# Optimization experiments

Measured on AMD Instinct MI355X. Metric: run time of the kernel, lower is better.

## Reference

```python
import jax, jax.numpy as jnp
import numpy as np

B, T, E, D = 64, 128, 4, 128
K = 4 * D  # ffn_hidden_dim
AUX_COEF = 0.01


def setup_inputs() -> dict:
    key = jax.random.key(0)
    ks = jax.random.split(key, 7)
    return {
        "x": jax.random.normal(ks[0], (B, T, D), dtype=jnp.float32),
        "expert_w1": jax.random.normal(ks[1], (T, E, D, K), dtype=jnp.float32) * 0.02,
        "expert_b1": jnp.zeros((T, E, K), dtype=jnp.float32),
        "expert_w2": jax.random.normal(ks[2], (T, E, K, D), dtype=jnp.float32) * 0.02,
        "expert_b2": jnp.zeros((T, E, D), dtype=jnp.float32),
        # router_train nn.Linear(D, E): store as [D, E] plus bias [E]
        "router_w": jax.random.normal(ks[3], (D, E), dtype=jnp.float32) * (1.0 / np.sqrt(D)),
        "router_b": jax.random.normal(ks[4], (E,), dtype=jnp.float32) * 0.01,
    }


def reference(x, expert_w1, expert_b1, expert_w2, expert_b2, router_w, router_b):
    # training=True path with use_relu_routing=True
    router_logits = jnp.einsum("btd,de->bte", x, router_w) + router_b  # [B,T,E]
    gates = jax.nn.relu(router_logits)
    gates = gates / (gates.sum(axis=-1, keepdims=True) + 1e-9)

    # per-token, per-expert 2-layer FFN
    hidden = jnp.einsum("btd,tedk->btek", x, expert_w1) + expert_b1  # [B,T,E,K]
    hidden = jax.nn.gelu(hidden, approximate=False)  # torch F.gelu default = exact erf
    expert_outputs = jnp.einsum("btek,tekd->bted", hidden, expert_w2) + expert_b2  # [B,T,E,D]

    output = (expert_outputs * gates[..., None]).sum(axis=2)  # [B,T,D]
    aux_loss = AUX_COEF * gates.sum() / (x.shape[0] * x.shape[1])
    return output, aux_loss
```

## Files before the change

### kernel.cpp

```cpp
#include <hip/hip_runtime.h>
#include <hip/hip_bf16.h>

#define NB 64
#define NT 128
#define NE 4
#define ND 128
#define NK 512

typedef __attribute__((ext_vector_type(8))) short bf16x8;
typedef __attribute__((ext_vector_type(4))) short bf16x4;
typedef __attribute__((ext_vector_type(4))) float f32x4;

__device__ __forceinline__ short f2bf(float f) {
    union { __hip_bfloat16 b; short s; } u;
    u.b = __float2bfloat16(f);
    return u.s;
}

__device__ __forceinline__ bf16x8 cvt8(const float* f) {
    bf16x8 r;
    #pragma unroll
    for (int j = 0; j < 8; ++j) r[j] = f2bf(f[j]);
    return r;
}

__device__ __forceinline__ bf16x4 cvt4(float4 f) {
    bf16x4 r;
    r[0] = f2bf(f.x); r[1] = f2bf(f.y); r[2] = f2bf(f.z); r[3] = f2bf(f.w);
    return r;
}

__device__ __forceinline__ float gelu_erf(float x) {
    return 0.5f * x * (1.0f + erff(x * 0.70710678118654752f));
}

__global__ __launch_bounds__(256)
void moe_gates(const float* __restrict__ x,
               const float* __restrict__ rw,
               const float* __restrict__ rb,
               float* __restrict__ gates_ws,
               float* __restrict__ aux_partial)
{
    const int tid  = threadIdx.x;
    const int lane = tid & 63;
    const int wave = tid >> 6;
    __shared__ float waux[4];

    const float4 rw0 = *(const float4*)(rw + lane * 4);
    const float4 rw1 = *(const float4*)(rw + (64 + lane) * 4);
    const float4 rbv = *(const float4*)rb;

    float aux = 0.f;
    #pragma unroll
    for (int i = 0; i < 4; ++i) {
        const int tok = (blockIdx.x * 4 + wave) * 4 + i;
        const float x0 = x[tok * ND + lane];
        const float x1 = x[tok * ND + 64 + lane];
        float p0 = x0 * rw0.x + x1 * rw1.x;
        float p1 = x0 * rw0.y + x1 * rw1.y;
        float p2 = x0 * rw0.z + x1 * rw1.z;
        float p3 = x0 * rw0.w + x1 * rw1.w;
        #pragma unroll
        for (int off = 32; off > 0; off >>= 1) {
            p0 += __shfl_xor(p0, off);
            p1 += __shfl_xor(p1, off);
            p2 += __shfl_xor(p2, off);
            p3 += __shfl_xor(p3, off);
        }
        if (lane == 0) {
            p0 = fmaxf(p0 + rbv.x, 0.f);
            p1 = fmaxf(p1 + rbv.y, 0.f);
            p2 = fmaxf(p2 + rbv.z, 0.f);
            p3 = fmaxf(p3 + rbv.w, 0.f);
            const float s   = p0 + p1 + p2 + p3;
            const float inv = 1.f / (s + 1e-9f);
            float4 g; g.x = p0 * inv; g.y = p1 * inv; g.z = p2 * inv; g.w = p3 * inv;
            *(float4*)(gates_ws + tok * NE) = g;
            aux += s * inv;
        }
    }
    if (lane == 0) waux[wave] = aux;
    __syncthreads();
    if (tid == 0)
        aux_partial[blockIdx.x] = waux[0] + waux[1] + waux[2] + waux[3];
}

__global__ __launch_bounds__(512, 4)
void moe_main(const float* __restrict__ x,
              const float* __restrict__ w1,
              const float* __restrict__ b1,
              const float* __restrict__ w2,
              const float* __restrict__ b2,
              const float* __restrict__ gates_ws,
              float* __restrict__ ws)
{
    const int bid  = blockIdx.x;
    const int t    = bid >> 2;
    const int e    = bid & 3;
    const int tid  = threadIdx.x;
    const int lane = tid & 63;
    const int wave = tid >> 6;
    const int l15  = lane & 15;
    const int l4   = lane >> 4;

    __shared__ __align__(16) char smem[66816];
    short* Hs     = (short*)smem;
    short* Xs     = (short*)smem;
    float* gate_s = (float*)(smem + 66560);

    if (tid < NB)
        gate_s[tid] = gates_ws[(tid * NT + t) * NE + e];

    {
        float4 xv[4];
        #pragma unroll
        for (int q = 0; q < 4; ++q) {
            const int f   = q * 512 + tid;
            const int row = f >> 5;
            const int c4  = f & 31;
            xv[q] = *(const float4*)(x + (size_t)(row * NT + t) * ND + c4 * 4);
        }
        #pragma unroll
        for (int q = 0; q < 4; ++q) {
            const int f   = q * 512 + tid;
            const int row = f >> 5;
            const int c4  = f & 31;
            *(bf16x4*)&Xs[row * 136 + c4 * 4] = cvt4(xv[q]);
        }
    }
    __syncthreads();

    const float* W1 = w1 + (size_t)((t * NE + e) * ND) * NK;
    const float* B1 = b1 + (t * NE + e) * NK;
    const int n0 = wave * 64;

    f32x4 acc[4][4];
    #pragma unroll
    for (int m = 0; m < 4; ++m)
        #pragma unroll
        for (int n = 0; n < 4; ++n) acc[m][n] = (f32x4){0.f, 0.f, 0.f, 0.f};

    {
        const float* wbase = W1 + (size_t)(l4 * 8) * NK + n0 + l15;
        float wbuf[4][8];
        #pragma unroll
        for (int q = 0; q < 4; ++q) {
            const float* wp = wbase + q * 16;
            #pragma unroll
            for (int j = 0; j < 8; ++j) wbuf[q][j] = wp[(size_t)j * NK];
        }

        bf16x8 afr[4];
        #pragma unroll
        for (int p = 0; p < 16; ++p) {
            const int ks = p >> 2, nt = p & 3;
            if (nt == 0) {
                const int d0 = ks * 32 + l4 * 8;
                #pragma unroll
                for (int m = 0; m < 4; ++m)
                    afr[m] = *(const bf16x8*)&Xs[(m * 16 + l15) * 136 + d0];
            }
            const bf16x8 bfr = cvt8(wbuf[p & 3]);
            if (p < 12) {
                const int p4 = p + 4;
                const int ks4 = p4 >> 2, nt4 = p4 & 3;
                const float* wp = wbase + (size_t)(ks4 * 32) * NK + nt4 * 16;
                #pragma unroll
                for (int j = 0; j < 8; ++j) wbuf[p4 & 3][j] = wp[(size_t)j * NK];
            }
            #pragma unroll
            for (int m = 0; m < 4; ++m)
                acc[m][nt] = __builtin_amdgcn_mfma_f32_16x16x32_bf16(afr[m], bfr, acc[m][nt], 0, 0, 0);
        }
    }
    __syncthreads();

    #pragma unroll
    for (int nt = 0; nt < 4; ++nt) {
        const int n = n0 + nt * 16 + l15;
        const float bb = B1[n];
        #pragma unroll
        for (int m = 0; m < 4; ++m) {
            const int row = m * 16 + l4 * 4;
            #pragma unroll
            for (int r = 0; r < 4; ++r) {
                const float hh = acc[m][nt][r] + bb;
                Hs[(row + r) * 520 + n] = f2bf(gelu_erf(hh));
            }
        }
    }
    __syncthreads();

    const float* W2 = w2 + (size_t)((t * NE + e) * NK) * ND;
    const float* B2 = b2 + (t * NE + e) * ND;
    const int c0 = wave * 16;

    f32x4 acc2[4];
    #pragma unroll
    for (int m = 0; m < 4; ++m) acc2[m] = (f32x4){0.f, 0.f, 0.f, 0.f};

    {
        const float* w2base = W2 + (size_t)(l4 * 8) * ND + c0 + l15;
        float wb2[4][8];
        #pragma unroll
        for (int q = 0; q < 4; ++q) {
            const float* wp = w2base + (size_t)(q * 32) * ND;
            #pragma unroll
            for (int j = 0; j < 8; ++j) wb2[q][j] = wp[(size_t)j * ND];
        }

        bf16x8 a2[4];
        #pragma unroll
        for (int p = 0; p < 16; ++p) {
            const int k0 = p * 32 + l4 * 8;
            #pragma unroll
            for (int m = 0; m < 4; ++m)
                a2[m] = *(const bf16x8*)(&Hs[(m * 16 + l15) * 520 + k0]);
            const bf16x8 bfr = cvt8(wb2[p & 3]);
            if (p < 12) {
                const int ks4 = p + 4;
                const float* wp = w2base + (size_t)(ks4 * 32) * ND;
                #pragma unroll
                for (int j = 0; j < 8; ++j) wb2[(p + 4) & 3][j] = wp[(size_t)j * ND];
            }
            #pragma unroll
            for (int m = 0; m < 4; ++m)
                acc2[m] = __builtin_amdgcn_mfma_f32_16x16x32_bf16(a2[m], bfr, acc2[m], 0, 0, 0);
        }
    }

    {
        const int c = c0 + l15;
        const float bb = B2[c];
        #pragma unroll
        for (int m = 0; m < 4; ++m) {
            #pragma unroll
            for (int r = 0; r < 4; ++r) {
                const int b = m * 16 + l4 * 4 + r;
                const float v = (acc2[m][r] + bb) * gate_s[b];
                ws[(size_t)(e * NB * NT + b * NT + t) * ND + c] = v;
            }
        }
    }
}

__global__ __launch_bounds__(256)
void moe_reduce(const float* __restrict__ ws,
                const float* __restrict__ aux_partial,
                float* __restrict__ out)
{
    const int i = blockIdx.x * blockDim.x + threadIdx.x;
    const int stride = NB * NT * ND / 4;
    const float4* w = (const float4*)ws;
    const float4 a = w[i];
    const float4 b = w[i + stride];
    const float4 c = w[i + 2 * stride];
    const float4 d = w[i + 3 * stride];
    float4 r;
    r.x = a.x + b.x + c.x + d.x;
    r.y = a.y + b.y + c.y + d.y;
    r.z = a.z + b.z + c.z + d.z;
    r.w = a.w + b.w + c.w + d.w;
    ((float4*)out)[i] = r;

    if (blockIdx.x == 0) {
        const int tid = threadIdx.x;
        float s = aux_partial[tid] + aux_partial[tid + 256];
        #pragma unroll
        for (int off = 32; off > 0; off >>= 1) s += __shfl_xor(s, off);
        __shared__ float wsum[4];
        if ((tid & 63) == 0) wsum[tid >> 6] = s;
        __syncthreads();
        if (tid == 0)
            out[NB * NT * ND] = (wsum[0] + wsum[1] + wsum[2] + wsum[3]) *
                                (0.01f / (NB * NT));
    }
}

__global__ __launch_bounds__(256, 2)
void moe_main_fb(const float* __restrict__ x,
                 const float* __restrict__ w1,
                 const float* __restrict__ b1,
                 const float* __restrict__ w2,
                 const float* __restrict__ b2,
                 const float* __restrict__ rw,
                 const float* __restrict__ rb,
                 float* __restrict__ out)
{
    const int blk  = blockIdx.x;
    const int t    = blk >> 2;
    const int e    = blk & 3;
    const int tid  = threadIdx.x;
    const int lane = tid & 63;
    const int wave = tid >> 6;
    const int l15  = lane & 15;
    const int l4   = lane >> 4;

    __shared__ short Hs[NB][NK + 8];
    __shared__ float gate_s[NB];

    if (tid < NB) {
        const int b = tid;
        const float* xr = x + (b * NT + t) * ND;
        float l0 = rb[0], l1 = rb[1], l2 = rb[2], l3 = rb[3];
        #pragma unroll 8
        for (int d = 0; d < ND; ++d) {
            const float xv = xr[d];
            const float* w = rw + d * NE;
            l0 += xv * w[0]; l1 += xv * w[1]; l2 += xv * w[2]; l3 += xv * w[3];
        }
        l0 = fmaxf(l0, 0.f); l1 = fmaxf(l1, 0.f); l2 = fmaxf(l2, 0.f); l3 = fmaxf(l3, 0.f);
        const float ss  = l0 + l1 + l2 + l3;
        const float inv = 1.f / (ss + 1e-9f);
        const float ge  = (e == 0) ? l0 : (e == 1) ? l1 : (e == 2) ? l2 : l3;
        gate_s[b] = ge * inv;
        if (e == 0) {
            float aux = ss * inv;
            #pragma unroll
            for (int off = 32; off > 0; off >>= 1) aux += __shfl_down(aux, off);
            if (lane == 0) atomicAdd(out + NB * NT * ND, aux * (0.01f / (NB * NT)));
        }
    }
    __syncthreads();

    const float* W1 = w1 + (size_t)((t * NE + e) * ND) * NK;
    const float* B1 = b1 + (t * NE + e) * NK;
    const int n0 = wave * 128;

    f32x4 acc[4][8];
    #pragma unroll
    for (int m = 0; m < 4; ++m)
        #pragma unroll
        for (int n = 0; n < 8; ++n) acc[m][n] = (f32x4){0.f, 0.f, 0.f, 0.f};

    #pragma unroll
    for (int ks = 0; ks < 4; ++ks) {
        const int d0 = ks * 32 + l4 * 8;
        bf16x8 afr[4];
        #pragma unroll
        for (int m = 0; m < 4; ++m) {
            const int b = m * 16 + l15;
            const float* xp = x + (b * NT + t) * ND + d0;
            float xf[8];
            *(float4*)&xf[0] = *(const float4*)(xp);
            *(float4*)&xf[4] = *(const float4*)(xp + 4);
            afr[m] = cvt8(xf);
        }
        #pragma unroll
        for (int nt = 0; nt < 8; ++nt) {
            const int n = n0 + nt * 16 + l15;
            const float* wp = W1 + (size_t)d0 * NK + n;
            float wf[8];
            #pragma unroll
            for (int j = 0; j < 8; ++j) wf[j] = wp[(size_t)j * NK];
            const bf16x8 bfr = cvt8(wf);
            #pragma unroll
            for (int m = 0; m < 4; ++m)
                acc[m][nt] = __builtin_amdgcn_mfma_f32_16x16x32_bf16(afr[m], bfr, acc[m][nt], 0, 0, 0);
        }
    }

    #pragma unroll
    for (int nt = 0; nt < 8; ++nt) {
        const int n = n0 + nt * 16 + l15;
        const float bb = B1[n];
        #pragma unroll
        for (int m = 0; m < 4; ++m) {
            const int row = m * 16 + l4 * 4;
            #pragma unroll
            for (int r = 0; r < 4; ++r) {
                const float hh = acc[m][nt][r] + bb;
                Hs[row + r][n] = f2bf(gelu_erf(hh));
            }
        }
    }
    __syncthreads();

    const float* W2 = w2 + (size_t)((t * NE + e) * NK) * ND;
    const float* B2 = b2 + (t * NE + e) * ND;
    const int c0 = wave * 32;

    f32x4 acc2[4][2];
    #pragma unroll
    for (int m = 0; m < 4; ++m)
        #pragma unroll
        for (int n = 0; n < 2; ++n) acc2[m][n] = (f32x4){0.f, 0.f, 0.f, 0.f};

    #pragma unroll 4
    for (int ks = 0; ks < 16; ++ks) {
        const int k0 = ks * 32 + l4 * 8;
        bf16x8 afr[4];
        #pragma unroll
        for (int m = 0; m < 4; ++m)
            afr[m] = *(const bf16x8*)(&Hs[m * 16 + l15][k0]);
        #pragma unroll
        for (int nt = 0; nt < 2; ++nt) {
            const int c = c0 + nt * 16 + l15;
            const float* wp = W2 + (size_t)k0 * ND + c;
            float wf[8];
            #pragma unroll
            for (int j = 0; j < 8; ++j) wf[j] = wp[(size_t)j * ND];
            const bf16x8 bfr = cvt8(wf);
            #pragma unroll
            for (int m = 0; m < 4; ++m)
                acc2[m][nt] = __builtin_amdgcn_mfma_f32_16x16x32_bf16(afr[m], bfr, acc2[m][nt], 0, 0, 0);
        }
    }

    #pragma unroll
    for (int nt = 0; nt < 2; ++nt) {
        const int c = c0 + nt * 16 + l15;
        const float bb = B2[c];
        #pragma unroll
        for (int m = 0; m < 4; ++m) {
            #pragma unroll
            for (int r = 0; r < 4; ++r) {
                const int b = m * 16 + l4 * 4 + r;
                const float v = (acc2[m][nt][r] + bb) * gate_s[b];
                atomicAdd(out + (size_t)(b * NT + t) * ND + c, v);
            }
        }
    }
}

extern "C" void kernel_launch(void* const* d_in, const int* in_sizes, int n_in,
                              void* d_out, int out_size, void* d_ws, size_t ws_size,
                              hipStream_t stream) {
    const float* x  = (const float*)d_in[0];
    const float* w1 = (const float*)d_in[1];
    const float* b1 = (const float*)d_in[2];
    const float* w2 = (const float*)d_in[3];
    const float* b2 = (const float*)d_in[4];
    const float* rw = (const float*)d_in[5];
    const float* rb = (const float*)d_in[6];
    float* out = (float*)d_out;

    const size_t contrib_elems = (size_t)NE * NB * NT * ND;
    const size_t gates_elems   = (size_t)NB * NT * NE;
    const size_t aux_elems     = 512;
    const size_t ws_need = (contrib_elems + gates_elems + aux_elems) * sizeof(float);

    if (ws_size >= ws_need) {
        float* contrib = (float*)d_ws;
        float* gates   = contrib + contrib_elems;
        float* auxp    = gates + gates_elems;

        moe_gates<<<512, 256, 0, stream>>>(x, rw, rb, gates, auxp);
        moe_main<<<NT * NE, 512, 0, stream>>>(x, w1, b1, w2, b2, gates, contrib);
        moe_reduce<<<(NB * NT * ND / 4) / 256, 256, 0, stream>>>(contrib, auxp, out);
    } else {
        hipMemsetAsync(d_out, 0, (size_t)(NB * NT * ND + 1) * sizeof(float), stream);
        moe_main_fb<<<NT * NE, 256, 0, stream>>>(x, w1, b1, w2, b2, rw, rb, out);
    }
}
```

Measured before the change: 62.46 us.

## Fuse expert-sum reduction into main kernel via per-token atomic tickets

Removes the separate reduce kernel launch. Each main block takes a per-token ticket with an atomic after a thread fence, and the last of the four expert blocks for a token sums the four contributions and writes the output. The block for token 0 also computes the aux loss. This trades one kernel launch and its dependency gap for an extra memset launch, atomics, fences, and a serial tail inside the last block for each token.

```diff
diff --git a/kernel.cpp b/kernel.cpp
--- a/kernel.cpp
+++ b/kernel.cpp
@@ -92,7 +92,10 @@
               const float* __restrict__ w2,
               const float* __restrict__ b2,
               const float* __restrict__ gates_ws,
-              float* __restrict__ ws)
+              float* __restrict__ ws,
+              const float* __restrict__ auxp,
+              int* __restrict__ tickets,
+              float* __restrict__ out)
 {
     const int bid  = blockIdx.x;
     const int t    = bid >> 2;
@@ -103,10 +106,12 @@
     const int l15  = lane & 15;
     const int l4   = lane >> 4;
 
-    __shared__ __align__(16) char smem[66816];
+    __shared__ __align__(16) char smem[66880];
     short* Hs     = (short*)smem;
     short* Xs     = (short*)smem;
     float* gate_s = (float*)(smem + 66560);
+    int*   last_s = (int*)(smem + 66816);
+    float* wsum   = (float*)(smem + 66820);
 
     if (tid < NB)
         gate_s[tid] = gates_ws[(tid * NT + t) * NE + e];
@@ -242,38 +247,47 @@
             }
         }
     }
-}
-
-__global__ __launch_bounds__(256)
-void moe_reduce(const float* __restrict__ ws,
-                const float* __restrict__ aux_partial,
-                float* __restrict__ out)
-{
-    const int i = blockIdx.x * blockDim.x + threadIdx.x;
-    const int stride = NB * NT * ND / 4;
-    const float4* w = (const float4*)ws;
-    const float4 a = w[i];
-    const float4 b = w[i + stride];
-    const float4 c = w[i + 2 * stride];
-    const float4 d = w[i + 3 * stride];
-    float4 r;
-    r.x = a.x + b.x + c.x + d.x;
-    r.y = a.y + b.y + c.y + d.y;
-    r.z = a.z + b.z + c.z + d.z;
-    r.w = a.w + b.w + c.w + d.w;
-    ((float4*)out)[i] = r;
-
-    if (blockIdx.x == 0) {
-        const int tid = threadIdx.x;
-        float s = aux_partial[tid] + aux_partial[tid + 256];
-        #pragma unroll
-        for (int off = 32; off > 0; off >>= 1) s += __shfl_xor(s, off);
-        __shared__ float wsum[4];
-        if ((tid & 63) == 0) wsum[tid >> 6] = s;
-        __syncthreads();
-        if (tid == 0)
-            out[NB * NT * ND] = (wsum[0] + wsum[1] + wsum[2] + wsum[3]) *
-                                (0.01f / (NB * NT));
+
+    __syncthreads();
+    if (tid == 0) {
+        __threadfence();
+        const int old = atomicAdd(&tickets[t], 1);
+        *last_s = (old == 3);
+    }
+    __syncthreads();
+    if (*last_s) {
+        __threadfence();
+        const size_t es = (size_t)NB * NT * ND;
+        #pragma unroll
+        for (int q = 0; q < 4; ++q) {
+            const int f  = q * 512 + tid;
+            const int b  = f >> 5;
+            const int d4 = f & 31;
+            const size_t base = ((size_t)(b * NT + t)) * ND + d4 * 4;
+            const float4 a0 = *(const float4*)(ws + base);
+            const float4 a1 = *(const float4*)(ws + es + base);
+            const float4 a2v = *(const float4*)(ws + 2 * es + base);
+            const float4 a3 = *(const float4*)(ws + 3 * es + base);
+            float4 r;
+            r.x = a0.x + a1.x + a2v.x + a3.x;
+            r.y = a0.y + a1.y + a2v.y + a3.y;
+            r.z = a0.z + a1.z + a2v.z + a3.z;
+            r.w = a0.w + a1.w + a2v.w + a3.w;
+            *(float4*)(out + base) = r;
+        }
+        if (t == 0) {
+            float s = auxp[tid];
+            #pragma unroll
+            for (int off = 32; off > 0; off >>= 1) s += __shfl_xor(s, off);
+            if (lane == 0) wsum[wave] = s;
+            __syncthreads();
+            if (tid == 0) {
+                float tot = 0.f;
+                #pragma unroll
+                for (int wv = 0; wv < 8; ++wv) tot += wsum[wv];
+                out[(size_t)NB * NT * ND] = tot * (0.01f / (NB * NT));
+            }
+        }
     }
 }
 
@@ -438,16 +452,20 @@
     const size_t contrib_elems = (size_t)NE * NB * NT * ND;
     const size_t gates_elems   = (size_t)NB * NT * NE;
     const size_t aux_elems     = 512;
-    const size_t ws_need = (contrib_elems + gates_elems + aux_elems) * sizeof(float);
+    const size_t ticket_elems  = NT;
+    const size_t ws_need = (contrib_elems + gates_elems + aux_elems) * sizeof(float)
+                         + ticket_elems * sizeof(int);
 
     if (ws_size >= ws_need) {
         float* contrib = (float*)d_ws;
         float* gates   = contrib + contrib_elems;
         float* auxp    = gates + gates_elems;
-
+        int*   tickets = (int*)(auxp + aux_elems);
+
+        hipMemsetAsync(tickets, 0, ticket_elems * sizeof(int), stream);
         moe_gates<<<512, 256, 0, stream>>>(x, rw, rb, gates, auxp);
-        moe_main<<<NT * NE, 512, 0, stream>>>(x, w1, b1, w2, b2, gates, contrib);
-        moe_reduce<<<(NB * NT * ND / 4) / 256, 256, 0, stream>>>(contrib, auxp, out);
+        moe_main<<<NT * NE, 512, 0, stream>>>(x, w1, b1, w2, b2, gates,
+                                              contrib, auxp, tickets, out);
     } else {
         hipMemsetAsync(d_out, 0, (size_t)(NB * NT * ND + 1) * sizeof(float), stream);
         moe_main_fb<<<NT * NE, 256, 0, stream>>>(x, w1, b1, w2, b2, rw, rb, out);
```

After: 171.5 us. 175% more time.
